# Performance work log

Measured on AMD Instinct MI355X. Metric: run time of the kernel, lower is better.

## Reference

```python
import jax, jax.numpy as jnp
import numpy as np

N, K, D = 2_000_000, 16, 3
EPS = 1e-6  # matches torch eye*1e-6 jitter added to the diagonal covariance


def setup_inputs() -> dict:
    key = jax.random.key(0)
    k1, k2, k3, k4 = jax.random.split(key, 4)
    x = jax.random.normal(k1, (N, D), dtype=jnp.float32)
    means = jax.random.normal(k2, (K, D), dtype=jnp.float32)
    # positive diagonal variances
    covariances = jax.random.uniform(k3, (K, D), dtype=jnp.float32, minval=0.5, maxval=2.0)
    w = jax.random.uniform(k4, (K,), dtype=jnp.float32, minval=0.1, maxval=1.0)
    weights = w / jnp.sum(w)  # mixture weights sum to 1
    return {"x": x, "means": means, "covariances": covariances, "weights": weights}


def reference(x, means, covariances, weights):
    # scale_tril of diag(cov)+eps*I is diag(sqrt(cov+eps))
    scale = jnp.sqrt(covariances + EPS)                      # [K, D]
    # standardized residuals: [N, K, D]
    z = (x[:, None, :] - means[None, :, :]) / scale[None, :, :]
    log_det = jnp.sum(jnp.log(scale), axis=-1)               # [K], log|L|
    d = x.shape[-1]
    # per-component Gaussian log-prob + log mixture weight: [N, K]
    log_prob = (-0.5 * (d * jnp.log(2.0 * jnp.pi) + jnp.sum(z * z, axis=-1))
                - log_det[None, :] + jnp.log(weights)[None, :])
    # mixture log-likelihood per point: [N]
    return jax.nn.logsumexp(log_prob, axis=1)
```

## Files before the change

### kernel.cpp

```cpp
#include <hip/hip_runtime.h>


constexpr int KCOMP = 16;
constexpr float EPS = 1e-6f;

__global__ __launch_bounds__(256) void gmm_loglik_kernel(
    const float* __restrict__ x,
    const float* __restrict__ means,
    const float* __restrict__ cov,
    const float* __restrict__ weights,
    float* __restrict__ out,
    int n)
{
    __shared__ float s_m0[KCOMP], s_m1[KCOMP], s_m2[KCOMP];
    __shared__ float s_h0[KCOMP], s_h1[KCOMP], s_h2[KCOMP];
    __shared__ float s_c[KCOMP];

    const int t = threadIdx.x;
    if (t < KCOMP) {
        float v0 = cov[t * 3 + 0] + EPS;
        float v1 = cov[t * 3 + 1] + EPS;
        float v2 = cov[t * 3 + 2] + EPS;
        s_m0[t] = means[t * 3 + 0];
        s_m1[t] = means[t * 3 + 1];
        s_m2[t] = means[t * 3 + 2];
        s_h0[t] = 0.5f / v0;
        s_h1[t] = 0.5f / v1;
        s_h2[t] = 0.5f / v2;
        s_c[t] = -2.7568155996140185f
                 - 0.5f * (__logf(v0) + __logf(v1) + __logf(v2))
                 + __logf(weights[t]);
    }
    __syncthreads();

    const int ngrp = n >> 2;
    const float4* __restrict__ x4 = (const float4*)x;
    float4* __restrict__ out4 = (float4*)out;
    const int stride = gridDim.x * blockDim.x;

    for (int g = blockIdx.x * blockDim.x + t; g < ngrp; g += stride) {
        float4 a = x4[3 * g + 0];
        float4 b = x4[3 * g + 1];
        float4 c = x4[3 * g + 2];
        float px[4] = {a.x, a.w, b.z, c.y};
        float py[4] = {a.y, b.x, b.w, c.z};
        float pz[4] = {a.z, b.y, c.x, c.w};
        float res[4];
#pragma unroll
        for (int p = 0; p < 4; ++p) {
            float lp[KCOMP];
            float mx = -3.4e38f;
#pragma unroll
            for (int k = 0; k < KCOMP; ++k) {
                float dx = px[p] - s_m0[k];
                float dy = py[p] - s_m1[k];
                float dz = pz[p] - s_m2[k];
                float q = dx * dx * s_h0[k];
                q += dy * dy * s_h1[k];
                q += dz * dz * s_h2[k];
                lp[k] = s_c[k] - q;
                mx = fmaxf(mx, lp[k]);
            }
            float s = 0.f;
#pragma unroll
            for (int k = 0; k < KCOMP; ++k)
                s += __expf(lp[k] - mx);
            res[p] = mx + __logf(s);
        }
        out4[g] = make_float4(res[0], res[1], res[2], res[3]);
    }

    const int tail_start = ngrp << 2;
    for (int i = tail_start + blockIdx.x * blockDim.x + t; i < n; i += stride) {
        float px = x[3 * i + 0], py = x[3 * i + 1], pz = x[3 * i + 2];
        float lp[KCOMP];
        float mx = -3.4e38f;
#pragma unroll
        for (int k = 0; k < KCOMP; ++k) {
            float dx = px - s_m0[k];
            float dy = py - s_m1[k];
            float dz = pz - s_m2[k];
            float q = dx * dx * s_h0[k] + dy * dy * s_h1[k] + dz * dz * s_h2[k];
            lp[k] = s_c[k] - q;
            mx = fmaxf(mx, lp[k]);
        }
        float s = 0.f;
#pragma unroll
        for (int k = 0; k < KCOMP; ++k)
            s += __expf(lp[k] - mx);
        out[i] = mx + __logf(s);
    }
}

extern "C" void kernel_launch(void* const* d_in, const int* in_sizes, int n_in,
                              void* d_out, int out_size, void* d_ws, size_t ws_size,
                              hipStream_t stream) {
    const float* x       = (const float*)d_in[0];
    const float* means   = (const float*)d_in[1];
    const float* cov     = (const float*)d_in[2];
    const float* weights = (const float*)d_in[3];
    float* out           = (float*)d_out;

    const int n = in_sizes[0] / 3;
    const int ngrp = n >> 2;
    int blocks = (ngrp + 255) / 256;
    if (blocks < 1) blocks = 1;

    gmm_loglik_kernel<<<blocks, 256, 0, stream>>>(x, means, cov, weights, out, n);
}
```

Baseline: 88.35 us.

## Expand quadratic into polynomial FMAs, use base-2 exp/log, split tail kernel

Expands each component's quadratic form into a per-component polynomial in X, Y, Z, X², Y², Z², so each component costs six FMAs against coefficients packed as float4 in shared memory. Coefficients are pre-scaled by log2(e) so exp2f/log2f replace __expf/__logf, avoiding per-element scaling. The grid-stride loop becomes one group per thread, and the remainder points move to a separate tail kernel, which may add a launch when n is not a multiple of four. The expanded form can lose some precision when means are far from the data.

```diff
diff --git a/kernel.cpp b/kernel.cpp
--- a/kernel.cpp
+++ b/kernel.cpp
@@ -3,6 +3,8 @@
 
 constexpr int KCOMP = 16;
 constexpr float EPS = 1e-6f;
+#define LOG2E 1.4426950408889634f
+#define LN2   0.6931471805599453f
 
 __global__ __launch_bounds__(256) void gmm_loglik_kernel(
     const float* __restrict__ x,
@@ -10,86 +12,102 @@
     const float* __restrict__ cov,
     const float* __restrict__ weights,
     float* __restrict__ out,
-    int n)
+    int ngrp)
 {
-    __shared__ float s_m0[KCOMP], s_m1[KCOMP], s_m2[KCOMP];
-    __shared__ float s_h0[KCOMP], s_h1[KCOMP], s_h2[KCOMP];
-    __shared__ float s_c[KCOMP];
+    __shared__ float4 s_cf[KCOMP * 2];
 
     const int t = threadIdx.x;
     if (t < KCOMP) {
-        float v0 = cov[t * 3 + 0] + EPS;
-        float v1 = cov[t * 3 + 1] + EPS;
-        float v2 = cov[t * 3 + 2] + EPS;
-        s_m0[t] = means[t * 3 + 0];
-        s_m1[t] = means[t * 3 + 1];
-        s_m2[t] = means[t * 3 + 2];
-        s_h0[t] = 0.5f / v0;
-        s_h1[t] = 0.5f / v1;
-        s_h2[t] = 0.5f / v2;
-        s_c[t] = -2.7568155996140185f
+        float v0 = cov[3 * t + 0] + EPS;
+        float v1 = cov[3 * t + 1] + EPS;
+        float v2 = cov[3 * t + 2] + EPS;
+        float m0 = means[3 * t + 0];
+        float m1 = means[3 * t + 1];
+        float m2 = means[3 * t + 2];
+        float h0 = 0.5f / v0, h1 = 0.5f / v1, h2 = 0.5f / v2;
+        float ck = -2.7568155996140185f
                  - 0.5f * (__logf(v0) + __logf(v1) + __logf(v2))
                  + __logf(weights[t]);
+        float A = ck - (h0 * m0 * m0 + h1 * m1 * m1 + h2 * m2 * m2);
+        s_cf[2 * t + 0] = make_float4(LOG2E * A,
+                                      LOG2E * 2.f * h0 * m0,
+                                      LOG2E * 2.f * h1 * m1,
+                                      LOG2E * 2.f * h2 * m2);
+        s_cf[2 * t + 1] = make_float4(-LOG2E * h0, -LOG2E * h1, -LOG2E * h2, 0.f);
     }
     __syncthreads();
 
-    const int ngrp = n >> 2;
+    const int g = blockIdx.x * blockDim.x + t;
+    if (g >= ngrp) return;
+
     const float4* __restrict__ x4 = (const float4*)x;
-    float4* __restrict__ out4 = (float4*)out;
-    const int stride = gridDim.x * blockDim.x;
+    float4 a = x4[3 * g + 0];
+    float4 b = x4[3 * g + 1];
+    float4 c = x4[3 * g + 2];
 
-    for (int g = blockIdx.x * blockDim.x + t; g < ngrp; g += stride) {
-        float4 a = x4[3 * g + 0];
-        float4 b = x4[3 * g + 1];
-        float4 c = x4[3 * g + 2];
-        float px[4] = {a.x, a.w, b.z, c.y};
-        float py[4] = {a.y, b.x, b.w, c.z};
-        float pz[4] = {a.z, b.y, c.x, c.w};
-        float res[4];
+    float px[4] = {a.x, a.w, b.z, c.y};
+    float py[4] = {a.y, b.x, b.w, c.z};
+    float pz[4] = {a.z, b.y, c.x, c.w};
+    float res[4];
+
 #pragma unroll
-        for (int p = 0; p < 4; ++p) {
-            float lp[KCOMP];
-            float mx = -3.4e38f;
-#pragma unroll
-            for (int k = 0; k < KCOMP; ++k) {
-                float dx = px[p] - s_m0[k];
-                float dy = py[p] - s_m1[k];
-                float dz = pz[p] - s_m2[k];
-                float q = dx * dx * s_h0[k];
-                q += dy * dy * s_h1[k];
-                q += dz * dz * s_h2[k];
-                lp[k] = s_c[k] - q;
-                mx = fmaxf(mx, lp[k]);
-            }
-            float s = 0.f;
-#pragma unroll
-            for (int k = 0; k < KCOMP; ++k)
-                s += __expf(lp[k] - mx);
-            res[p] = mx + __logf(s);
-        }
-        out4[g] = make_float4(res[0], res[1], res[2], res[3]);
-    }
-
-    const int tail_start = ngrp << 2;
-    for (int i = tail_start + blockIdx.x * blockDim.x + t; i < n; i += stride) {
-        float px = x[3 * i + 0], py = x[3 * i + 1], pz = x[3 * i + 2];
+    for (int p = 0; p < 4; ++p) {
+        const float X = px[p], Y = py[p], Z = pz[p];
+        const float X2 = X * X, Y2 = Y * Y, Z2 = Z * Z;
         float lp[KCOMP];
         float mx = -3.4e38f;
 #pragma unroll
         for (int k = 0; k < KCOMP; ++k) {
-            float dx = px - s_m0[k];
-            float dy = py - s_m1[k];
-            float dz = pz - s_m2[k];
-            float q = dx * dx * s_h0[k] + dy * dy * s_h1[k] + dz * dz * s_h2[k];
-            lp[k] = s_c[k] - q;
-            mx = fmaxf(mx, lp[k]);
+            float4 u = s_cf[2 * k + 0];
+            float4 v = s_cf[2 * k + 1];
+            float q = fmaf(u.y, X, u.x);
+            q = fmaf(u.z, Y, q);
+            q = fmaf(u.w, Z, q);
+            q = fmaf(v.x, X2, q);
+            q = fmaf(v.y, Y2, q);
+            q = fmaf(v.z, Z2, q);
+            lp[k] = q;
+            mx = fmaxf(mx, q);
         }
         float s = 0.f;
 #pragma unroll
         for (int k = 0; k < KCOMP; ++k)
-            s += __expf(lp[k] - mx);
-        out[i] = mx + __logf(s);
+            s += exp2f(lp[k] - mx);
+        res[p] = LN2 * (mx + log2f(s));
     }
+
+    ((float4*)out)[g] = make_float4(res[0], res[1], res[2], res[3]);
+}
+
+__global__ void gmm_tail_kernel(
+    const float* __restrict__ x,
+    const float* __restrict__ means,
+    const float* __restrict__ cov,
+    const float* __restrict__ weights,
+    float* __restrict__ out,
+    int start, int n)
+{
+    int i = start + blockIdx.x * blockDim.x + threadIdx.x;
+    if (i >= n) return;
+    float X = x[3 * i], Y = x[3 * i + 1], Z = x[3 * i + 2];
+    float lp[KCOMP];
+    float mx = -3.4e38f;
+#pragma unroll
+    for (int k = 0; k < KCOMP; ++k) {
+        float v0 = cov[3 * k] + EPS, v1 = cov[3 * k + 1] + EPS, v2 = cov[3 * k + 2] + EPS;
+        float dx = X - means[3 * k], dy = Y - means[3 * k + 1], dz = Z - means[3 * k + 2];
+        float q = -2.7568155996140185f
+                - 0.5f * (__logf(v0) + __logf(v1) + __logf(v2))
+                + __logf(weights[k])
+                - 0.5f * (dx * dx / v0 + dy * dy / v1 + dz * dz / v2);
+        lp[k] = q;
+        mx = fmaxf(mx, q);
+    }
+    float s = 0.f;
+#pragma unroll
+    for (int k = 0; k < KCOMP; ++k)
+        s += __expf(lp[k] - mx);
+    out[i] = mx + __logf(s);
 }
 
 extern "C" void kernel_launch(void* const* d_in, const int* in_sizes, int n_in,
@@ -103,8 +121,12 @@
 
     const int n = in_sizes[0] / 3;
     const int ngrp = n >> 2;
-    int blocks = (ngrp + 255) / 256;
-    if (blocks < 1) blocks = 1;
-
-    gmm_loglik_kernel<<<blocks, 256, 0, stream>>>(x, means, cov, weights, out, n);
+    if (ngrp > 0) {
+        int blocks = (ngrp + 255) / 256;
+        gmm_loglik_kernel<<<blocks, 256, 0, stream>>>(x, means, cov, weights, out, ngrp);
+    }
+    const int rem = n - (ngrp << 2);
+    if (rem > 0) {
+        gmm_tail_kernel<<<1, 64, 0, stream>>>(x, means, cov, weights, out, ngrp << 2, n);
+    }
 }
```

Result: faster. 84.49 us (-4.4%).
